# Kernel tuning notes

Hardware: AMD Instinct MI355X
Metric: run time of the kernel (lower is better)

Reference implementation:

```python
import jax, jax.numpy as jnp
import numpy as np

DIM = 1024
HEADS = 16
HEAD_DIM = DIM // HEADS
SCALE = HEAD_DIM ** -0.5
EPS_R = 1e-8
EPS_LN = 1e-5


def setup_inputs() -> dict:
    key = jax.random.key(0)
    ks = jax.random.split(key, 8)
    B, L = 4, 2048
    tokens = jax.random.normal(ks[0], (B, L, DIM), dtype=jnp.float32)
    R = jax.random.uniform(ks[1], (L, L), dtype=jnp.float32)
    s = DIM ** -0.5
    Wq = jax.random.normal(ks[2], (DIM, DIM), dtype=jnp.float32) * s
    Wk = jax.random.normal(ks[3], (DIM, DIM), dtype=jnp.float32) * s
    Wv = jax.random.normal(ks[4], (DIM, DIM), dtype=jnp.float32) * s
    Wp = jax.random.normal(ks[5], (DIM, DIM), dtype=jnp.float32) * s
    beta = jnp.ones((1,), dtype=jnp.float32)
    gamma = jnp.ones((DIM,), dtype=jnp.float32)
    bias = jnp.zeros((DIM,), dtype=jnp.float32)
    return {"tokens": tokens, "R": R, "Wq": Wq, "Wk": Wk, "Wv": Wv,
            "Wp": Wp, "beta": beta, "gamma": gamma, "bias": bias}


def reference(tokens, R, Wq, Wk, Wv, Wp, beta, gamma, bias):
    B, L, D = tokens.shape
    H, Dh = HEADS, HEAD_DIM
    residual = tokens
    # nn.Linear(bias=False): y = x @ W.T
    Q = (tokens @ Wq.T).reshape(B, L, H, Dh).transpose(0, 2, 1, 3)  # [B,H,L,Dh]
    K = (tokens @ Wk.T).reshape(B, L, H, Dh).transpose(0, 2, 1, 3)
    V = (tokens @ Wv.T).reshape(B, L, H, Dh).transpose(0, 2, 1, 3)
    attn = jnp.einsum('bhqd,bhkd->bhqk', Q, K) * SCALE
    log_R = jnp.log(jnp.maximum(R, EPS_R))  # [L,L]
    attn = attn + beta[0] * log_R[None, None, :, :]
    attn = jax.nn.softmax(attn, axis=-1)
    out = jnp.einsum('bhqk,bhkd->bhqd', attn, V)
    out = out.transpose(0, 2, 1, 3).reshape(B, L, D)
    out = out @ Wp.T
    x = out + residual
    mu = jnp.mean(x, axis=-1, keepdims=True)
    var = jnp.mean(jnp.square(x - mu), axis=-1, keepdims=True)
    return (x - mu) * jax.lax.rsqrt(var + EPS_LN) * gamma + bias
```

## Files before the change

### kernel.cpp

```cpp
#include <hip/hip_runtime.h>

#define DEV __device__ __forceinline__

typedef __attribute__((ext_vector_type(4))) float f32x4;
typedef __attribute__((ext_vector_type(16))) float f32x16;
typedef __attribute__((ext_vector_type(8))) short bf8v;
typedef __attribute__((ext_vector_type(4))) unsigned short u16x4;
typedef __attribute__((ext_vector_type(8))) unsigned short u16x8;
typedef __attribute__((ext_vector_type(2))) unsigned int u32x2;

static constexpr int LSEQ = 2048;
static constexpr int DIM  = 1024;
static constexpr int NH   = 16;
static constexpr int DH   = 64;
static constexpr int NB   = 4;
static constexpr int MROWS = NB * LSEQ;
static constexpr float QSCALE = 0.18033688011112042f;

DEV unsigned short f2bf(float x) {
  unsigned u = __float_as_uint(x);
  return (unsigned short)((u + 0x7fffu + ((u >> 16) & 1u)) >> 16);
}

DEV unsigned cvt_pk_bf16(float a, float b) {
  unsigned r;
  asm("v_cvt_pk_bf16_f32 %0, %1, %2" : "=v"(r) : "v"(a), "v"(b));
  return r;
}

DEV void pl32swap(unsigned& a, unsigned& b) {
  asm("v_permlane32_swap_b32 %0, %1" : "+v"(a), "+v"(b));
}

DEV float fexp2(float x) {
  float r;
  asm("v_exp_f32 %0, %1" : "=v"(r) : "v"(x));
  return r;
}

DEV void gload_lds16(const void* g, void* l) {
  __builtin_amdgcn_global_load_lds((const __attribute__((address_space(1))) void*)g,
                                   (__attribute__((address_space(3))) void*)l, 16, 0, 0);
}

__global__ __launch_bounds__(256) void k_cvt(const float* __restrict__ src,
                                             unsigned short* __restrict__ dst, int n) {
  int i = (blockIdx.x * 256 + threadIdx.x) * 8;
  if (i >= n) return;
  f32x4 a = *(const f32x4*)(src + i);
  f32x4 b = *(const f32x4*)(src + i + 4);
  u16x8 o;
  o[0] = f2bf(a[0]); o[1] = f2bf(a[1]); o[2] = f2bf(a[2]); o[3] = f2bf(a[3]);
  o[4] = f2bf(b[0]); o[5] = f2bf(b[1]); o[6] = f2bf(b[2]); o[7] = f2bf(b[3]);
  *(u16x8*)(dst + i) = o;
}

__global__ __launch_bounds__(256) void k_rbq(const float* __restrict__ R,
                                             const float* __restrict__ beta,
                                             u16x4* __restrict__ out) {
  __shared__ u16x4 lds[32 * 128];
  const int tid = threadIdx.x;
  const int q0 = blockIdx.x * 128, k0 = blockIdx.y * 128;
  const float b = beta[0];
  #pragma unroll
  for (int i = 0; i < 8; ++i) {
    int row = i * 16 + (tid >> 4);
    int col = (tid & 15) * 8;
    const float* src = R + (size_t)(q0 + row) * 2048 + k0 + col;
    f32x4 v0 = *(const f32x4*)src;
    f32x4 v1 = *(const f32x4*)(src + 4);
    u16x4 qa, qb;
    #pragma unroll
    for (int m = 0; m < 4; ++m) {
      qa[m] = f2bf(exp2f(b * log2f(fmaxf(v0[m], 1e-8f))));
      qb[m] = f2bf(exp2f(b * log2f(fmaxf(v1[m], 1e-8f))));
    }
    lds[(col >> 2) * 128 + row] = qa;
    lds[((col >> 2) + 1) * 128 + row] = qb;
  }
  __syncthreads();
  const int qd_l = tid >> 3;
  const int qs = (tid & 7) * 16;
  #pragma unroll
  for (int j = 0; j < 16; ++j)
    out[(size_t)((k0 >> 2) + qd_l) * 2048 + q0 + qs + j] = lds[qd_l * 128 + qs + j];
}

DEV void gemm_core(const unsigned short* __restrict__ A, const unsigned short* __restrict__ Bm,
                   int m0, int n0, unsigned short* As, unsigned short* Bs, f32x4 (*acc)[4]) {
  const int tid = threadIdx.x;
  const int lane = tid & 63, wid = tid >> 6;
  const int g = lane >> 4, lq = lane & 15;
  const int wr = wid >> 1, wc = wid & 1;

  int aoff[2][4], boff[2][4];
  #pragma unroll
  for (int kk = 0; kk < 2; ++kk) {
    #pragma unroll
    for (int t = 0; t < 4; ++t) {
      aoff[kk][t] = (((wr * 64 + t * 16 + lq) * 128 + kk * 64 + g * 16) ^ ((lq & 7) << 4));
      boff[kk][t] = (((wc * 64 + t * 16 + lq) * 128 + kk * 64 + g * 16) ^ ((lq & 7) << 4));
    }
  }

  for (int kt = 0; kt < 16; ++kt) {
    #pragma unroll
    for (int i = 0; i < 4; ++i) {
      int chunk = i * 256 + tid;
      int row = chunk >> 3;
      int cc = (chunk & 7) ^ (row & 7);
      gload_lds16(A + (size_t)(m0 + row) * 1024 + kt * 64 + cc * 8, As + (i * 256 + wid * 64) * 8);
      gload_lds16(Bm + (size_t)(n0 + row) * 1024 + kt * 64 + cc * 8, Bs + (i * 256 + wid * 64) * 8);
    }
    __syncthreads();
    #pragma unroll
    for (int kk = 0; kk < 2; ++kk) {
      bf8v af[4], bfr[4];
      #pragma unroll
      for (int mi = 0; mi < 4; ++mi) af[mi] = *(const bf8v*)((const char*)As + aoff[kk][mi]);
      #pragma unroll
      for (int ni = 0; ni < 4; ++ni) bfr[ni] = *(const bf8v*)((const char*)Bs + boff[kk][ni]);
      #pragma unroll
      for (int mi = 0; mi < 4; ++mi)
        #pragma unroll
        for (int ni = 0; ni < 4; ++ni)
          acc[mi][ni] = __builtin_amdgcn_mfma_f32_16x16x32_bf16(af[mi], bfr[ni], acc[mi][ni], 0, 0, 0);
    }
    __syncthreads();
  }
}

__global__ __launch_bounds__(256) void k_gemm_qkv(
    const unsigned short* __restrict__ A, const unsigned short* __restrict__ W,
    unsigned short* __restrict__ Qb, unsigned short* __restrict__ Kb,
    unsigned short* __restrict__ Vt) {
  __shared__ unsigned short As[128 * 64];
  __shared__ unsigned short Bs[128 * 64];
  f32x4 acc[4][4];
  f32x4 z = {0.f, 0.f, 0.f, 0.f};
  #pragma unroll
  for (int mi = 0; mi < 4; ++mi)
    #pragma unroll
    for (int ni = 0; ni < 4; ++ni) acc[mi][ni] = z;

  const int m0 = blockIdx.x * 128, n0 = blockIdx.y * 128;
  gemm_core(A, W, m0, n0, As, Bs, acc);

  const int tid = threadIdx.x;
  const int lane = tid & 63, wid = tid >> 6;
  const int g = lane >> 4, lq = lane & 15;
  const int wr = wid >> 1, wc = wid & 1;
  const int region = n0 >> 10;
  const int nrel0 = n0 & 1023;

  if (region < 2) {
    unsigned short* dst = (region == 0) ? Qb : Kb;
    const float sc = (region == 0) ? QSCALE : 1.0f;
    #pragma unroll
    for (int mi = 0; mi < 4; ++mi)
      #pragma unroll
      for (int ni = 0; ni < 4; ++ni) {
        int m = m0 + wr * 64 + mi * 16 + g * 4;
        int n = nrel0 + wc * 64 + ni * 16 + lq;
        int b = m >> 11, l = m & 2047;
        int h = n >> 6, d = n & 63;
        int base = ((b * NH + h) * LSEQ + l) * DH + d;
        #pragma unroll
        for (int r = 0; r < 4; ++r)
          dst[base + r * DH] = f2bf(acc[mi][ni][r] * sc);
      }
  } else {
    #pragma unroll
    for (int mi = 0; mi < 4; ++mi)
      #pragma unroll
      for (int ni = 0; ni < 4; ++ni) {
        int m = m0 + wr * 64 + mi * 16 + g * 4;
        int n = nrel0 + wc * 64 + ni * 16 + lq;
        int b = m >> 11, l = m & 2047;
        int h = n >> 6, d = n & 63;
        u16x4 pk;
        #pragma unroll
        for (int r = 0; r < 4; ++r) pk[r] = f2bf(acc[mi][ni][r]);
        *(u16x4*)(Vt + (size_t)((b * NH + h) * DH + d) * LSEQ + l) = pk;
      }
  }
}

__global__ __launch_bounds__(256, 4) void k_attn(
    const unsigned short* __restrict__ Qb, const unsigned short* __restrict__ Kb,
    const unsigned short* __restrict__ Vt, const u16x4* __restrict__ RbQ,
    unsigned short* __restrict__ AO) {
  __shared__ unsigned short Ks[2][64 * 64];
  __shared__ unsigned short Vs[2][64 * 64];
  const int tid = threadIdx.x;
  const int lane = tid & 63, wid = tid >> 6;
  const int l32 = lane & 31, hi = lane >> 5;
  const int bh = blockIdx.y;
  const int q0 = blockIdx.x * 128;
  const int b = bh >> 4, h = bh & 15;
  const unsigned short* Qbh = Qb + (size_t)bh * LSEQ * DH;
  const unsigned short* Kbh = Kb + (size_t)bh * LSEQ * DH;
  const unsigned short* Vbh = Vt + (size_t)bh * DH * LSEQ;
  const int qw = q0 + wid * 32;
  const int q = qw + l32;

  bf8v qf[4];
  #pragma unroll
  for (int s = 0; s < 4; ++s)
    qf[s] = *(const bf8v*)(Qbh + (size_t)q * DH + s * 16 + hi * 8);

  f32x16 oacc[2];
  #pragma unroll
  for (int db = 0; db < 2; ++db)
    #pragma unroll
    for (int r = 0; r < 16; ++r) oacc[db][r] = 0.f;
  float mrun = -__builtin_inff();
  float lrun = 0.f;

  const u16x4* rq = RbQ + q;

  #pragma unroll
  for (int i = 0; i < 2; ++i) {
    int chunk = i * 256 + tid;
    int row = chunk >> 3;
    int cc = (chunk & 7) ^ (row & 7);
    gload_lds16(Kbh + (size_t)row * DH + cc * 8, &Ks[0][(i * 256 + wid * 64) * 8]);
    gload_lds16(Vbh + (size_t)row * LSEQ + cc * 8, &Vs[0][(i * 256 + wid * 64) * 8]);
  }
  __syncthreads();

  auto TILE = [&](int t, int buf, bool pref) {
    u16x4 rb[8];
    #pragma unroll
    for (int s2 = 0; s2 < 8; ++s2)
      rb[s2] = rq[(size_t)(t * 16 + 2 * s2 + hi) * 2048];

    if (pref) {
      #pragma unroll
      for (int i = 0; i < 2; ++i) {
        int chunk = i * 256 + tid;
        int row = chunk >> 3;
        int cc = (chunk & 7) ^ (row & 7);
        gload_lds16(Kbh + (size_t)((t + 1) * 64 + row) * DH + cc * 8,
                    &Ks[buf ^ 1][(i * 256 + wid * 64) * 8]);
        gload_lds16(Vbh + (size_t)row * LSEQ + (t + 1) * 64 + cc * 8,
                    &Vs[buf ^ 1][(i * 256 + wid * 64) * 8]);
      }
    }

    f32x16 sac[2];
    #pragma unroll
    for (int r = 0; r < 16; ++r) { sac[0][r] = 0.f; sac[1][r] = 0.f; }
    __builtin_amdgcn_s_setprio(1);
    #pragma unroll
    for (int s = 0; s < 4; ++s) {
      #pragma unroll
      for (int kb2 = 0; kb2 < 2; ++kb2) {
        int row = kb2 * 32 + l32;
        bf8v kf = *(const bf8v*)((const char*)Ks[buf] +
                   ((row * 128 + s * 32 + hi * 16) ^ ((row & 7) << 4)));
        sac[kb2] = __builtin_amdgcn_mfma_f32_32x32x16_bf16(kf, qf[s], sac[kb2], 0, 0, 0);
      }
    }
    __builtin_amdgcn_s_setprio(0);

    float mx;
    {
      float m8[8];
      #pragma unroll
      for (int j = 0; j < 8; ++j)
        m8[j] = fmaxf(fmaxf(sac[0][2 * j], sac[0][2 * j + 1]),
                      fmaxf(sac[1][2 * j], sac[1][2 * j + 1]));
      float m4a = fmaxf(m8[0], m8[1]), m4b = fmaxf(m8[2], m8[3]);
      float m4c = fmaxf(m8[4], m8[5]), m4d = fmaxf(m8[6], m8[7]);
      mx = fmaxf(fmaxf(m4a, m4b), fmaxf(m4c, m4d));
      mx = fmaxf(mx, __shfl_xor(mx, 32));
    }

    if (__any(mx > mrun + 8.f)) {
      float mnew = fmaxf(mrun, mx);
      float corr = fexp2(mrun - mnew);
      mrun = mnew;
      lrun *= corr;
      #pragma unroll
      for (int db = 0; db < 2; ++db)
        #pragma unroll
        for (int r = 0; r < 16; ++r) oacc[db][r] *= corr;
    }

    float ls = 0.f;
    auto SLICE = [&](int s) {
      const int blk = s >> 1, r0 = 8 * (s & 1);
      const u16x4 ra = rb[2 * s], rc = rb[2 * s + 1];
      float p[8];
      #pragma unroll
      for (int i = 0; i < 4; ++i) {
        float rf = __uint_as_float((unsigned)ra[i] << 16);
        p[i] = fexp2(sac[blk][r0 + i] - mrun) * rf;
      }
      #pragma unroll
      for (int i = 0; i < 4; ++i) {
        float rf = __uint_as_float((unsigned)rc[i] << 16);
        p[4 + i] = fexp2(sac[blk][r0 + 4 + i] - mrun) * rf;
      }
      ls += ((p[0] + p[1]) + (p[2] + p[3])) + ((p[4] + p[5]) + (p[6] + p[7]));
      unsigned w0 = cvt_pk_bf16(p[0], p[1]);
      unsigned w2 = cvt_pk_bf16(p[4], p[5]);
      unsigned w1 = cvt_pk_bf16(p[2], p[3]);
      unsigned w3 = cvt_pk_bf16(p[6], p[7]);
      pl32swap(w0, w2);
      pl32swap(w1, w3);
      union { unsigned w[4]; bf8v v; } pf;
      pf.w[0] = w0; pf.w[1] = w1; pf.w[2] = w2; pf.w[3] = w3;
      #pragma unroll
      for (int db = 0; db < 2; ++db) {
        int row = db * 32 + l32;
        bf8v vf = *(const bf8v*)((const char*)Vs[buf] +
                   ((row * 128 + s * 32 + hi * 16) ^ ((row & 7) << 4)));
        oacc[db] = __builtin_amdgcn_mfma_f32_32x32x16_bf16(vf, pf.v, oacc[db], 0, 0, 0);
      }
    };
    SLICE(0); SLICE(1); SLICE(2); SLICE(3);
    ls += __shfl_xor(ls, 32);
    lrun += ls;
    __syncthreads();
  };

  for (int tp = 0; tp < 16; ++tp) {
    TILE(2 * tp,     0, true);
    TILE(2 * tp + 1, 1, tp != 15);
  }

  float inv = 1.f / lrun;
  #pragma unroll
  for (int db = 0; db < 2; ++db)
    #pragma unroll
    for (int u = 0; u < 4; ++u) {
      u32x2 w;
      w[0] = cvt_pk_bf16(oacc[db][4 * u + 0] * inv, oacc[db][4 * u + 1] * inv);
      w[1] = cvt_pk_bf16(oacc[db][4 * u + 2] * inv, oacc[db][4 * u + 3] * inv);
      int d = db * 32 + u * 8 + hi * 4;
      *(u32x2*)(AO + (size_t)(b * LSEQ + q) * DIM + h * DH + d) = w;
    }
}

__global__ __launch_bounds__(256) void k_gemm_proj(
    const unsigned short* __restrict__ A, const unsigned short* __restrict__ W,
    const float* __restrict__ res, float* __restrict__ out) {
  __shared__ unsigned short As[128 * 64];
  __shared__ unsigned short Bs[128 * 64];
  f32x4 acc[4][4];
  f32x4 z = {0.f, 0.f, 0.f, 0.f};
  #pragma unroll
  for (int mi = 0; mi < 4; ++mi)
    #pragma unroll
    for (int ni = 0; ni < 4; ++ni) acc[mi][ni] = z;

  const int m0 = blockIdx.x * 128, n0 = blockIdx.y * 128;
  gemm_core(A, W, m0, n0, As, Bs, acc);

  const int tid = threadIdx.x;
  const int lane = tid & 63, wid = tid >> 6;
  const int g = lane >> 4, lq = lane & 15;
  const int wr = wid >> 1, wc = wid & 1;
  #pragma unroll
  for (int mi = 0; mi < 4; ++mi)
    #pragma unroll
    for (int ni = 0; ni < 4; ++ni) {
      int m = m0 + wr * 64 + mi * 16 + g * 4;
      int n = n0 + wc * 64 + ni * 16 + lq;
      #pragma unroll
      for (int r = 0; r < 4; ++r) {
        int idx = (m + r) * 1024 + n;
        out[idx] = acc[mi][ni][r] + res[idx];
      }
    }
}

__global__ __launch_bounds__(256) void k_ln(float* __restrict__ x,
                                            const float* __restrict__ gamma,
                                            const float* __restrict__ bias) {
  const int row = blockIdx.x;
  const int tid = threadIdx.x;
  float* xr = x + (size_t)row * 1024;
  f32x4 v = *(f32x4*)(xr + tid * 4);
  float s = v[0] + v[1] + v[2] + v[3];
  float ss = v[0] * v[0] + v[1] * v[1] + v[2] * v[2] + v[3] * v[3];
  #pragma unroll
  for (int off = 1; off < 64; off <<= 1) {
    s += __shfl_xor(s, off);
    ss += __shfl_xor(ss, off);
  }
  __shared__ float red[8];
  const int lane = tid & 63, wid = tid >> 6;
  if (lane == 0) { red[wid] = s; red[wid + 4] = ss; }
  __syncthreads();
  s = red[0] + red[1] + red[2] + red[3];
  ss = red[4] + red[5] + red[6] + red[7];
  float mu = s * (1.f / 1024.f);
  float var = ss * (1.f / 1024.f) - mu * mu;
  float rs = rsqrtf(var + 1e-5f);
  f32x4 gm = *(const f32x4*)(gamma + tid * 4);
  f32x4 bi = *(const f32x4*)(bias + tid * 4);
  f32x4 o;
  #pragma unroll
  for (int j = 0; j < 4; ++j) o[j] = (v[j] - mu) * rs * gm[j] + bi[j];
  *(f32x4*)(xr + tid * 4) = o;
}

extern "C" void kernel_launch(void* const* d_in, const int* in_sizes, int n_in,
                              void* d_out, int out_size, void* d_ws, size_t ws_size,
                              hipStream_t stream) {
  const float* tokens = (const float*)d_in[0];
  const float* R      = (const float*)d_in[1];
  const float* Wq     = (const float*)d_in[2];
  const float* Wk     = (const float*)d_in[3];
  const float* Wv     = (const float*)d_in[4];
  const float* Wp     = (const float*)d_in[5];
  const float* beta   = (const float*)d_in[6];
  const float* gamma  = (const float*)d_in[7];
  const float* bias   = (const float*)d_in[8];
  float* out = (float*)d_out;
  char* ws = (char*)d_ws;

  unsigned short* tok_bf = (unsigned short*)(ws);
  unsigned short* wqkv   = (unsigned short*)(ws + 16777216);
  unsigned short* wp     = (unsigned short*)(ws + 23068672);
  u16x4*          rbq    = (u16x4*)(ws + 25165824);
  unsigned short* qb     = (unsigned short*)(ws + 41943040);
  unsigned short* kb     = (unsigned short*)(ws + 58720256);
  unsigned short* vt     = (unsigned short*)(ws + 75497472);
  unsigned short* ao     = tok_bf;

  k_cvt<<<4096, 256, 0, stream>>>(tokens, tok_bf, MROWS * DIM);
  k_cvt<<<512, 256, 0, stream>>>(Wq, wqkv, DIM * DIM);
  k_cvt<<<512, 256, 0, stream>>>(Wk, wqkv + DIM * DIM, DIM * DIM);
  k_cvt<<<512, 256, 0, stream>>>(Wv, wqkv + 2 * DIM * DIM, DIM * DIM);
  k_cvt<<<512, 256, 0, stream>>>(Wp, wp, DIM * DIM);
  k_rbq<<<dim3(16, 16), 256, 0, stream>>>(R, beta, rbq);

  k_gemm_qkv<<<dim3(64, 24), 256, 0, stream>>>(tok_bf, wqkv, qb, kb, vt);
  k_attn<<<dim3(16, 64), 256, 0, stream>>>(qb, kb, vt, rbq, ao);
  k_gemm_proj<<<dim3(64, 8), 256, 0, stream>>>(ao, wp, tokens, out);
  k_ln<<<8192, 256, 0, stream>>>(out, gamma, bias);
}
```

Baseline: 264.3 us.

## Reorder R-bias table so each lane loads contiguous 64-byte rows per tile

Changes the precomputed exp(beta*log R) bf16 table layout so that, for each 64-key tile, each query's 32 needed values for its half-lane sit contiguously. The attention kernel then issues four 16-byte vector loads per tile instead of eight strided 8-byte loads spaced 16 KB apart. The preprocessing kernel is retiled (128x64 blocks, padded LDS) to produce the new layout. This aims to cut memory transactions and TLB/cache pressure on the bias reads in the attention loop.

```diff
diff --git a/kernel.cpp b/kernel.cpp
--- a/kernel.cpp
+++ b/kernel.cpp
@@ -55,18 +55,19 @@
   *(u16x8*)(dst + i) = o;
 }
 
-__global__ __launch_bounds__(256) void k_rbq(const float* __restrict__ R,
+__global__ __launch_bounds__(256) void k_rbt(const float* __restrict__ R,
                                              const float* __restrict__ beta,
                                              u16x4* __restrict__ out) {
-  __shared__ u16x4 lds[32 * 128];
-  const int tid = threadIdx.x;
-  const int q0 = blockIdx.x * 128, k0 = blockIdx.y * 128;
+  __shared__ u16x4 lds[128][17];
+  const int tid = threadIdx.x;
+  const int q0 = blockIdx.x * 128;
+  const int k0 = blockIdx.y * 64;
   const float b = beta[0];
   #pragma unroll
-  for (int i = 0; i < 8; ++i) {
-    int row = i * 16 + (tid >> 4);
-    int col = (tid & 15) * 8;
-    const float* src = R + (size_t)(q0 + row) * 2048 + k0 + col;
+  for (int it = 0; it < 4; ++it) {
+    int ql = it * 32 + (tid >> 3);
+    int kl = (tid & 7) * 8;
+    const float* src = R + (size_t)(q0 + ql) * 2048 + k0 + kl;
     f32x4 v0 = *(const f32x4*)src;
     f32x4 v1 = *(const f32x4*)(src + 4);
     u16x4 qa, qb;
@@ -75,15 +76,17 @@
       qa[m] = f2bf(exp2f(b * log2f(fmaxf(v0[m], 1e-8f))));
       qb[m] = f2bf(exp2f(b * log2f(fmaxf(v1[m], 1e-8f))));
     }
-    lds[(col >> 2) * 128 + row] = qa;
-    lds[((col >> 2) + 1) * 128 + row] = qb;
+    int qd = kl >> 2;
+    lds[ql][(qd & 1) * 8 + (qd >> 1)] = qa;
+    lds[ql][((qd + 1) & 1) * 8 + ((qd + 1) >> 1)] = qb;
   }
   __syncthreads();
-  const int qd_l = tid >> 3;
-  const int qs = (tid & 7) * 16;
-  #pragma unroll
-  for (int j = 0; j < 16; ++j)
-    out[(size_t)((k0 >> 2) + qd_l) * 2048 + q0 + qs + j] = lds[qd_l * 128 + qs + j];
+  u16x4* o = out + ((size_t)blockIdx.y * 2048 + q0) * 16;
+  #pragma unroll
+  for (int j = 0; j < 8; ++j) {
+    int idx = tid * 8 + j;
+    o[idx] = lds[idx >> 4][idx & 15];
+  }
 }
 
 DEV void gemm_core(const unsigned short* __restrict__ A, const unsigned short* __restrict__ Bm,
@@ -188,7 +191,7 @@
 
 __global__ __launch_bounds__(256, 4) void k_attn(
     const unsigned short* __restrict__ Qb, const unsigned short* __restrict__ Kb,
-    const unsigned short* __restrict__ Vt, const u16x4* __restrict__ RbQ,
+    const unsigned short* __restrict__ Vt, const unsigned short* __restrict__ RbT,
     unsigned short* __restrict__ AO) {
   __shared__ unsigned short Ks[2][64 * 64];
   __shared__ unsigned short Vs[2][64 * 64];
@@ -217,7 +220,7 @@
   float mrun = -__builtin_inff();
   float lrun = 0.f;
 
-  const u16x4* rq = RbQ + q;
+  const char* rbp0 = (const char*)RbT + ((size_t)q * 2 + hi) * 64;
 
   #pragma unroll
   for (int i = 0; i < 2; ++i) {
@@ -230,10 +233,12 @@
   __syncthreads();
 
   auto TILE = [&](int t, int buf, bool pref) {
-    u16x4 rb[8];
-    #pragma unroll
-    for (int s2 = 0; s2 < 8; ++s2)
-      rb[s2] = rq[(size_t)(t * 16 + 2 * s2 + hi) * 2048];
+    const char* rbp = rbp0 + (size_t)t * (2048 * 128);
+    u16x8 rr[4];
+    rr[0] = *(const u16x8*)(rbp);
+    rr[1] = *(const u16x8*)(rbp + 16);
+    rr[2] = *(const u16x8*)(rbp + 32);
+    rr[3] = *(const u16x8*)(rbp + 48);
 
     if (pref) {
       #pragma unroll
@@ -291,17 +296,12 @@
     float ls = 0.f;
     auto SLICE = [&](int s) {
       const int blk = s >> 1, r0 = 8 * (s & 1);
-      const u16x4 ra = rb[2 * s], rc = rb[2 * s + 1];
+      const u16x8 rv = rr[s];
       float p[8];
       #pragma unroll
-      for (int i = 0; i < 4; ++i) {
-        float rf = __uint_as_float((unsigned)ra[i] << 16);
+      for (int i = 0; i < 8; ++i) {
+        float rf = __uint_as_float((unsigned)(unsigned short)rv[i] << 16);
         p[i] = fexp2(sac[blk][r0 + i] - mrun) * rf;
-      }
-      #pragma unroll
-      for (int i = 0; i < 4; ++i) {
-        float rf = __uint_as_float((unsigned)rc[i] << 16);
-        p[4 + i] = fexp2(sac[blk][r0 + 4 + i] - mrun) * rf;
       }
       ls += ((p[0] + p[1]) + (p[2] + p[3])) + ((p[4] + p[5]) + (p[6] + p[7]));
       unsigned w0 = cvt_pk_bf16(p[0], p[1]);
@@ -426,7 +426,7 @@
   unsigned short* tok_bf = (unsigned short*)(ws);
   unsigned short* wqkv   = (unsigned short*)(ws + 16777216);
   unsigned short* wp     = (unsigned short*)(ws + 23068672);
-  u16x4*          rbq    = (u16x4*)(ws + 25165824);
+  u16x4*          rbt    = (u16x4*)(ws + 25165824);
   unsigned short* qb     = (unsigned short*)(ws + 41943040);
   unsigned short* kb     = (unsigned short*)(ws + 58720256);
   unsigned short* vt     = (unsigned short*)(ws + 75497472);
@@ -437,10 +437,10 @@
   k_cvt<<<512, 256, 0, stream>>>(Wk, wqkv + DIM * DIM, DIM * DIM);
   k_cvt<<<512, 256, 0, stream>>>(Wv, wqkv + 2 * DIM * DIM, DIM * DIM);
   k_cvt<<<512, 256, 0, stream>>>(Wp, wp, DIM * DIM);
-  k_rbq<<<dim3(16, 16), 256, 0, stream>>>(R, beta, rbq);
+  k_rbt<<<dim3(16, 32), 256, 0, stream>>>(R, beta, rbt);
 
   k_gemm_qkv<<<dim3(64, 24), 256, 0, stream>>>(tok_bf, wqkv, qb, kb, vt);
-  k_attn<<<dim3(16, 64), 256, 0, stream>>>(qb, kb, vt, rbq, ao);
+  k_attn<<<dim3(16, 64), 256, 0, stream>>>(qb, kb, vt, (const unsigned short*)rbt, ao);
   k_gemm_proj<<<dim3(64, 8), 256, 0, stream>>>(ao, wp, tokens, out);
   k_ln<<<8192, 256, 0, stream>>>(out, gamma, bias);
 }
```

Measured after the change: 278.9 us. +5.5%, slower.
